# Performance work log

Hardware: AMD Instinct MI355X
Metric: run time of the kernel (lower is better)

The kernel has to match this reference:

```python
import jax, jax.numpy as jnp
import numpy as np

# ---- config (mirrors AAModel init kwargs: ns=48, nv=10, sh_lmax=1) ----
N, E, NS, NV = 100000, 60000, 48, 10
SED, DED = 32, 32          # sigma / distance embedding dims
CUTOFF = 30.0              # GaussianSmearing(0, cutoff, DED)
SQ3 = float(np.sqrt(3.0))
W1_NUMEL = NS * NS + NS * NV                                   # 2784
# layer-2 fully-connected TP path weight offsets:
#   0e(x)0e->0e, 0e(x)1o->1o, 1o(x)0e->1o, 1o(x)1o->0e, 1o(x)1o->1e
O2 = [2304, 2784, 2884, 3364, 3464]


def _mlp2(x, W1, b1, W2, b2):
    return jax.nn.relu(x @ W1 + b1) @ W2 + b2


def _seg_mean(x, idx, n):
    s = jax.ops.segment_sum(x, idx, num_segments=n)
    cnt = jax.ops.segment_sum(jnp.ones(idx.shape, x.dtype), idx, num_segments=n)
    return s / jnp.maximum(cnt, 1.0).reshape((n,) + (1,) * (x.ndim - 1))


def _forward(pos, node_sigma_emb, node_s, edge_W1, edge_b1, edge_W2, edge_b2,
             fc1_W1, fc1_b1, fc1_W2, fc1_b2, fc2_W1, fc2_b1, fc2_W2, fc2_b2,
             edge_index):
    src, dst = edge_index[0], edge_index[1]
    vec = pos[dst] - pos[src]                          # [E,3]
    d = jnp.linalg.norm(vec, axis=-1)                  # [E]
    sh1 = SQ3 * vec / (d[:, None] + 1e-8)              # l=1 SH, component norm; sh0 == 1
    # Gaussian smearing of edge distances
    offsets = jnp.linspace(0.0, CUTOFF, DED)
    coeff = -0.5 / (offsets[1] - offsets[0]) ** 2
    demb = jnp.exp(coeff * (d[:, None] - offsets) ** 2)          # [E,DED]
    edge_emb = _mlp2(jnp.concatenate([node_sigma_emb[src], demb], -1),
                     edge_W1, edge_b1, edge_W2, edge_b2)         # [E,NS]

    # ---- conv layer 1:  ns x0e  (x)  1x0e+1x1o  ->  ns x0e + nv x1o ----
    xs = node_s[src]
    ea = jnp.concatenate([edge_emb, node_s[src], node_s[dst]], -1)   # [E,3*NS]
    w = _mlp2(ea, fc1_W1, fc1_b1, fc1_W2, fc1_b2)                    # [E,2784]
    w00 = w[:, :NS * NS].reshape(-1, NS, NS)
    w01 = w[:, NS * NS:].reshape(-1, NS, NV)
    inv = 1.0 / np.sqrt(NS)
    m_s = jnp.einsum('eio,ei->eo', w00, xs) * inv                    # [E,NS]
    m_v = jnp.einsum('eio,ei->eo', w01, xs)[:, :, None] * sh1[:, None, :] * inv  # [E,NV,3]
    node_s1 = node_s + _seg_mean(m_s, dst, N)                        # residual
    node_v1 = _seg_mean(m_v, dst, N)

    # ---- conv layer 2:  ns x0e + nv x1o  (x)  1x0e+1x1o  ->  ns x0e + nv x1o + nv x1e ----
    ea2 = jnp.concatenate([edge_emb, node_s1[src], node_s1[dst]], -1)
    w2 = _mlp2(ea2, fc2_W1, fc2_b1, fc2_W2, fc2_b2)                  # [E,3464]
    w00 = w2[:, :O2[0]].reshape(-1, NS, NS)
    w01 = w2[:, O2[0]:O2[1]].reshape(-1, NS, NV)
    w10 = w2[:, O2[1]:O2[2]].reshape(-1, NV, NV)
    w11s = w2[:, O2[2]:O2[3]].reshape(-1, NV, NS)
    w11p = w2[:, O2[3]:O2[4]].reshape(-1, NV, NV)
    xs, xv = node_s1[src], node_v1[src]
    nA = 1.0 / np.sqrt(2 * NS)
    nB = 1.0 / np.sqrt(2 * NV)
    m_s = (jnp.einsum('eio,ei->eo', w00, xs) * nA
           + jnp.einsum('eio,eid,ed->eo', w11s, xv, sh1) * (nB / SQ3))
    m_v = (jnp.einsum('eio,ei->eo', w01, xs)[:, :, None] * sh1[:, None, :] * nA
           + jnp.einsum('eio,eid->eod', w10, xv) * nB)
    m_p = jnp.einsum('eio,eid->eod', w11p, jnp.cross(xv, sh1[:, None, :])) * (1.0 / np.sqrt(2.0 * NV))
    node_s2 = node_s1 + _seg_mean(m_s, dst, N)
    node_v2 = node_v1 + _seg_mean(m_v, dst, N)
    node_p = _seg_mean(m_p, dst, N)
    # final node irreps ns x0e + nv x1o + nv x1e, flattened -> [N, 108]
    return jnp.concatenate([node_s2, node_v2.reshape(N, -1), node_p.reshape(N, -1)], -1)


def setup_inputs() -> dict:
    key = jax.random.key(0)
    k = jax.random.split(key, 10)
    f32 = jnp.float32
    def lin(kk, fi, fo):
        return jax.random.normal(kk, (fi, fo), f32) / np.sqrt(fi)
    return {
        'pos': 10.0 * jax.random.normal(k[0], (N, 3), f32),
        'node_sigma_emb': jax.random.normal(k[1], (N, SED), f32),
        'node_s': jax.random.normal(k[2], (N, NS), f32),
        'edge_W1': lin(k[3], SED + DED, NS), 'edge_b1': jnp.zeros((NS,), f32),
        'edge_W2': lin(k[4], NS, NS), 'edge_b2': jnp.zeros((NS,), f32),
        'fc1_W1': lin(k[5], 3 * NS, 3 * NS), 'fc1_b1': jnp.zeros((3 * NS,), f32),
        'fc1_W2': lin(k[6], 3 * NS, W1_NUMEL), 'fc1_b2': jnp.zeros((W1_NUMEL,), f32),
        'fc2_W1': lin(k[7], 3 * NS, 3 * NS), 'fc2_b1': jnp.zeros((3 * NS,), f32),
        'fc2_W2': lin(k[8], 3 * NS, O2[-1]), 'fc2_b2': jnp.zeros((O2[-1],), f32),
        'edge_index': jax.random.randint(k[9], (2, E), 0, N, jnp.int32),
    }


def reference(pos, node_sigma_emb, node_s, edge_W1, edge_b1, edge_W2, edge_b2,
              fc1_W1, fc1_b1, fc1_W2, fc1_b2, fc2_W1, fc2_b1, fc2_W2, fc2_b2,
              edge_index):
    return _forward(pos, node_sigma_emb, node_s, edge_W1, edge_b1, edge_W2, edge_b2,
                    fc1_W1, fc1_b1, fc1_W2, fc1_b2, fc2_W1, fc2_b1, fc2_W2, fc2_b2,
                    edge_index)
```

## Files before the change

### kernel.cpp

```cpp
#include <hip/hip_runtime.h>
#include <math.h>


constexpr float SQ3f = 1.7320508075688772f;
constexpr float INV1 = 0.14433756729740643f;
constexpr float NAc  = 0.10206207261596575f;
constexpr float NBc  = 0.22360679774997896f;
constexpr float C20  = 0.22360679774997896f;
constexpr float RATIO= 1.2649110640673518f;
constexpr float DSP  = 30.0f/31.0f;
constexpr float GCOEF= -0.5f/(DSP*DSP);

typedef __attribute__((ext_vector_type(8))) short bf16x8;
typedef __attribute__((ext_vector_type(4))) float f32x4;

__device__ __forceinline__ unsigned short f2bf(float x) {
    unsigned u = __builtin_bit_cast(unsigned, x);
    u += 0x7fffu + ((u >> 16) & 1u);
    return (unsigned short)(u >> 16);
}

__device__ __forceinline__ int colmap(int layer, int t, int lm) {
    if (layer == 0) return t*16 + lm;
    if (layer == 1) {
        if (t < 144) { const int og=t/48, i=t-og*48; return i*48 + og*16 + lm; }
        const int i = t-144; return (lm<10) ? 2304 + i*10 + lm : -1;
    }
    if (t < 144) { const int og=t/48, i=t-og*48; return i*48 + og*16 + lm; }
    if (t < 174) { const int s=t-144, og=s/10, i=s-og*10; return 2884 + i*48 + og*16 + lm; }
    if (t < 222) { const int i=t-174; return (lm<10) ? 2304 + i*10 + lm : -1; }
    if (t < 232) { const int i=t-222; return (lm<10) ? 2784 + i*10 + lm : -1; }
    { const int i=t-232; return (lm<10) ? 3364 + i*10 + lm : -1; }
}

__global__ __launch_bounds__(256)
void cvt_swz(const float* __restrict__ W, const float* __restrict__ bias,
             short* __restrict__ Wsw, int ncol, int ntile, int layer)
{
    const int gid = blockIdx.x*256 + threadIdx.x;
    const int g = gid >> 6, lane = gid & 63;
    if (g >= ntile*5) return;
    const int tile = g/5, ks = g - tile*5;
    const int c  = colmap(layer, tile, lane & 15);
    const int k0 = ks*32 + (lane >> 4)*8;
    union { uint4 u4; unsigned short h[8]; } pk;
    #pragma unroll
    for (int j=0;j<8;j++) {
        const int k = k0 + j;
        float v = 0.f;
        if (c >= 0) {
            if (k < 144)       v = W[(size_t)k*ncol + c];
            else if (k == 144) v = bias[c];
        }
        pk.h[j] = f2bf(v);
    }
    *(uint4*)&Wsw[((size_t)g*64 + lane)*8] = pk.u4;
}

__global__ __launch_bounds__(256)
void edge_kernel(const float* __restrict__ pos, const float* __restrict__ sigma,
                 const int* __restrict__ ei,
                 const float* __restrict__ W1, const float* __restrict__ b1,
                 const float* __restrict__ W2, const float* __restrict__ b2,
                 float* __restrict__ edge_emb, float* __restrict__ sh1buf,
                 int* __restrict__ deg, int E)
{
    __shared__ float inl[4][64];
    __shared__ float hidl[4][48];
    const int w    = threadIdx.x >> 6;
    const int lane = threadIdx.x & 63;
    const int e    = blockIdx.x*4 + w;
    const bool valid = (e < E);
    const int ec = valid ? e : 0;
    const int src = ei[ec], dst = ei[E+ec];
    const float vx = pos[dst*3+0]-pos[src*3+0];
    const float vy = pos[dst*3+1]-pos[src*3+1];
    const float vz = pos[dst*3+2]-pos[src*3+2];
    const float d  = sqrtf(vx*vx+vy*vy+vz*vz);
    const float si = SQ3f/(d+1e-8f);
    const float s0 = vx*si, s1 = vy*si, s2 = vz*si;
    if (lane < 32) {
        inl[w][lane] = sigma[src*32+lane];
    } else {
        const float off  = (float)(lane-32)*DSP;
        const float diff = d - off;
        inl[w][lane] = expf(GCOEF*diff*diff);
    }
    __syncthreads();
    if (lane < 48) {
        float a = b1[lane];
        #pragma unroll 8
        for (int j=0;j<64;j++) a = fmaf(inl[w][j], W1[j*48+lane], a);
        hidl[w][lane] = fmaxf(a, 0.f);
    }
    __syncthreads();
    if (valid) {
        if (lane < 48) {
            float a = b2[lane];
            #pragma unroll 8
            for (int j=0;j<48;j++) a = fmaf(hidl[w][j], W2[j*48+lane], a);
            edge_emb[e*48+lane] = a;
        }
        if (lane == 0) atomicAdd(&deg[dst], 1);
        if (lane < 3)  sh1buf[e*4+lane] = (lane==0)?s0:((lane==1)?s1:s2);
    }
}

__device__ __forceinline__ void load_bfrag(const short* __restrict__ Wsw,
                                           int tile, int lane, bf16x8 (&b)[5]) {
    #pragma unroll
    for (int ks=0; ks<5; ks++)
        b[ks] = *(const bf16x8*)&Wsw[((size_t)(tile*5+ks)*64 + lane)*8];
}

template<typename F>
__device__ __forceinline__ void region1(const short* __restrict__ Wsw, int base,
                                        int count, int lane,
                                        const bf16x8 (&ag)[4][5], F&& upd)
{
    bf16x8 bc[5], bn[5];
    load_bfrag(Wsw, base, lane, bc);
    for (int i=0; i<count; ++i) {
        if (i+1 < count) load_bfrag(Wsw, base+i+1, lane, bn);
        f32x4 a[4];
        #pragma unroll
        for (int mt=0; mt<4; mt++) a[mt] = (f32x4){0.f,0.f,0.f,0.f};
        #pragma unroll
        for (int ks=0; ks<5; ks++)
            #pragma unroll
            for (int mt=0; mt<4; mt++)
                a[mt] = __builtin_amdgcn_mfma_f32_16x16x32_bf16(ag[mt][ks], bc[ks], a[mt], 0,0,0);
        upd(i, a);
        #pragma unroll
        for (int ks=0; ks<5; ks++) bc[ks] = bn[ks];
    }
}

template<int LAYER>
__global__ __launch_bounds__(256)
void conv_kernel(const float* __restrict__ edge_emb, const float* __restrict__ sh1buf,
                 const int* __restrict__ ei,
                 const float* __restrict__ sin_, const float* __restrict__ vin,
                 const short* __restrict__ W1sw, const short* __restrict__ W2sw,
                 float* __restrict__ outS, float* __restrict__ outV, int E)
{
    __shared__ __align__(16) short pool[64*192];
    __shared__ __align__(16) float xsT[48][68];
    __shared__ float sh1l[64][4];
    __shared__ int   srcl[64], dstl[64];
    __shared__ __align__(16) float xvT[LAYER==2 ? 30 : 1][68];
    __shared__ __align__(16) float uT [LAYER==2 ? 10 : 1][68];
    __shared__ __align__(16) float cvT[LAYER==2 ? 30 : 1][68];

    const int t  = threadIdx.x;
    const int eb = blockIdx.x * 64;

    if (t < 64) {
        const int ge = eb + t; const int gc = (ge < E) ? ge : (E-1);
        srcl[t] = ei[gc]; dstl[t] = ei[E+gc];
    }
    {
        const int e = t >> 2, k = t & 3;
        const int ge = eb + e; const int gc = (ge<E)?ge:(E-1);
        sh1l[e][k] = sh1buf[gc*4 + k];
    }
    __syncthreads();

    for (int p = t; p < 64*24; p += 256) {
        const int m = p / 24, s = p - m*24;
        const int k0 = s*8;
        float vals[8] = {0.f,0.f,0.f,0.f,0.f,0.f,0.f,0.f};
        if (k0 < 48) {
            const int ge = eb + m; const int gc = (ge<E)?ge:(E-1);
            const float4 a = *(const float4*)&edge_emb[gc*48 + k0];
            const float4 b = *(const float4*)&edge_emb[gc*48 + k0 + 4];
            vals[0]=a.x; vals[1]=a.y; vals[2]=a.z; vals[3]=a.w;
            vals[4]=b.x; vals[5]=b.y; vals[6]=b.z; vals[7]=b.w;
        } else if (k0 < 96) {
            const float4 a = *(const float4*)&sin_[srcl[m]*48 + (k0-48)];
            const float4 b = *(const float4*)&sin_[srcl[m]*48 + (k0-48) + 4];
            vals[0]=a.x; vals[1]=a.y; vals[2]=a.z; vals[3]=a.w;
            vals[4]=b.x; vals[5]=b.y; vals[6]=b.z; vals[7]=b.w;
            #pragma unroll
            for (int j=0;j<8;j++) xsT[k0-48+j][m] = vals[j];
        } else if (k0 < 144) {
            const float4 a = *(const float4*)&sin_[dstl[m]*48 + (k0-96)];
            const float4 b = *(const float4*)&sin_[dstl[m]*48 + (k0-96) + 4];
            vals[0]=a.x; vals[1]=a.y; vals[2]=a.z; vals[3]=a.w;
            vals[4]=b.x; vals[5]=b.y; vals[6]=b.z; vals[7]=b.w;
        } else if (k0 == 144) {
            vals[0] = 1.f;
        }
        union { uint4 u4; unsigned short h[8]; } pk;
        #pragma unroll
        for (int j=0;j<8;j++) pk.h[j] = f2bf(vals[j]);
        *(uint4*)&pool[m*192 + ((s ^ (m&7))*8)] = pk.u4;
    }
    if (LAYER==2) {
        for (int p=t; p<640; p+=256) {
            const int i = p >> 6, e = p & 63;
            const float x0 = vin[srcl[e]*30 + i*3+0];
            const float x1 = vin[srcl[e]*30 + i*3+1];
            const float x2 = vin[srcl[e]*30 + i*3+2];
            const float h0=sh1l[e][0], h1=sh1l[e][1], h2=sh1l[e][2];
            xvT[i*3+0][e]=x0; xvT[i*3+1][e]=x1; xvT[i*3+2][e]=x2;
            uT[i][e] = x0*h0 + x1*h1 + x2*h2;
            cvT[i*3+0][e] = x1*h2 - x2*h1;
            cvT[i*3+1][e] = x2*h0 - x0*h2;
            cvT[i*3+2][e] = x0*h1 - x1*h0;
        }
    }
    __syncthreads();

    const int wv = t >> 6, lane = t & 63;
    const int lm = lane & 15, lk = lane >> 4, lk4 = lk*4;

    {
        bf16x8 af[4][5];
        #pragma unroll
        for (int mt=0; mt<4; mt++) {
            const int m = mt*16 + lm;
            #pragma unroll
            for (int ks=0; ks<5; ks++)
                af[mt][ks] = *(const bf16x8*)&pool[m*192 + (((ks*4+lk) ^ (m&7))*8)];
        }
        f32x4 acc[3][4];
        #pragma unroll
        for (int j=0; j<3; j++) {
            const int nt = wv + j*4;
            if (nt < 9) {
                bf16x8 bw[5];
                load_bfrag(W1sw, nt, lane, bw);
                #pragma unroll
                for (int mt=0; mt<4; mt++) acc[j][mt] = (f32x4){0.f,0.f,0.f,0.f};
                #pragma unroll
                for (int ks=0; ks<5; ks++)
                    #pragma unroll
                    for (int mt=0; mt<4; mt++)
                        acc[j][mt] = __builtin_amdgcn_mfma_f32_16x16x32_bf16(af[mt][ks], bw[ks], acc[j][mt], 0,0,0);
            }
        }
        __syncthreads();
        #pragma unroll
        for (int j=0; j<3; j++) {
            const int nt = wv + j*4;
            if (nt < 9) {
                const int c = nt*16 + lm;
                #pragma unroll
                for (int mt=0; mt<4; mt++)
                    #pragma unroll
                    for (int r=0; r<4; r++) {
                        const int m = mt*16 + lk4 + r;
                        pool[m*192 + (((c>>3) ^ (m&7))*8) + (c&7)] = (short)f2bf(fmaxf(acc[j][mt][r], 0.f));
                    }
            }
        }
        if (t < 128) {
            const int m = t >> 1, s = 18 + (t & 1);
            union { uint4 u4; unsigned short h[8]; } pk;
            pk.u4.x = pk.u4.y = pk.u4.z = pk.u4.w = 0u;
            if (s == 18) pk.h[0] = f2bf(1.f);
            *(uint4*)&pool[m*192 + ((s ^ (m&7))*8)] = pk.u4;
        }
    }
    __syncthreads();

    bf16x8 ag[4][5];
    #pragma unroll
    for (int mt=0; mt<4; mt++) {
        const int m = mt*16 + lm;
        #pragma unroll
        for (int ks=0; ks<5; ks++)
            ag[mt][ks] = *(const bf16x8*)&pool[m*192 + (((ks*4+lk) ^ (m&7))*8)];
    }

    if (wv < 3) {
        float ms[4][4] = {};
        region1(W2sw, wv*48, 48, lane, ag, [&](int i, const f32x4 (&a)[4]) {
            #pragma unroll
            for (int mt=0; mt<4; mt++) {
                const f32x4 x = *(const f32x4*)&xsT[i][mt*16 + lk4];
                #pragma unroll
                for (int r=0;r<4;r++) ms[mt][r] = fmaf(a[mt][r], x[r], ms[mt][r]);
            }
        });
        if (LAYER==2) {
            region1(W2sw, 144 + wv*10, 10, lane, ag, [&](int i, const f32x4 (&a)[4]) {
                #pragma unroll
                for (int mt=0; mt<4; mt++) {
                    const f32x4 u = *(const f32x4*)&uT[i][mt*16 + lk4];
                    #pragma unroll
                    for (int r=0;r<4;r++) ms[mt][r] = fmaf(a[mt][r]*RATIO, u[r], ms[mt][r]);
                }
            });
        }
        const float scale = (LAYER==1) ? INV1 : NAc;
        const int   strd  = (LAYER==1) ? 48 : 108;
        const int o = wv*16 + lm;
        #pragma unroll
        for (int mt=0; mt<4; mt++)
            #pragma unroll
            for (int r=0;r<4;r++) {
                const int e = mt*16 + lk4 + r;
                if (eb+e < E) unsafeAtomicAdd(&outS[(size_t)dstl[e]*strd + o], ms[mt][r]*scale);
            }
    } else {
        float vc[4][4] = {};
        region1(W2sw, (LAYER==1) ? 144 : 174, 48, lane, ag, [&](int i, const f32x4 (&a)[4]) {
            #pragma unroll
            for (int mt=0; mt<4; mt++) {
                const f32x4 x = *(const f32x4*)&xsT[i][mt*16 + lk4];
                #pragma unroll
                for (int r=0;r<4;r++) vc[mt][r] = fmaf(a[mt][r], x[r], vc[mt][r]);
            }
        });
        if (LAYER==1) {
            if (lm < 10) {
                #pragma unroll
                for (int mt=0; mt<4; mt++)
                    #pragma unroll
                    for (int r=0;r<4;r++) {
                        const int e = mt*16 + lk4 + r;
                        if (eb+e < E) {
                            const float v = vc[mt][r]*INV1;
                            #pragma unroll
                            for (int d=0; d<3; d++)
                                unsafeAtomicAdd(&outV[(size_t)dstl[e]*30 + lm*3 + d], v*sh1l[e][d]);
                        }
                    }
            }
        } else {
            {
                float m3[4][4][3] = {};
                region1(W2sw, 222, 10, lane, ag, [&](int i, const f32x4 (&a)[4]) {
                    #pragma unroll
                    for (int d=0; d<3; d++)
                        #pragma unroll
                        for (int mt=0; mt<4; mt++) {
                            const f32x4 x = *(const f32x4*)&xvT[i*3+d][mt*16 + lk4];
                            #pragma unroll
                            for (int r=0;r<4;r++) m3[mt][r][d] = fmaf(a[mt][r], x[r], m3[mt][r][d]);
                        }
                });
                if (lm < 10) {
                    #pragma unroll
                    for (int mt=0; mt<4; mt++)
                        #pragma unroll
                        for (int r=0;r<4;r++) {
                            const int e = mt*16 + lk4 + r;
                            if (eb+e < E) {
                                const float v = vc[mt][r]*NAc;
                                #pragma unroll
                                for (int d=0; d<3; d++)
                                    unsafeAtomicAdd(&outS[(size_t)dstl[e]*108 + 48 + lm*3 + d],
                                                    v*sh1l[e][d] + m3[mt][r][d]*NBc);
                            }
                        }
                }
            }
            {
                float m3[4][4][3] = {};
                region1(W2sw, 232, 10, lane, ag, [&](int i, const f32x4 (&a)[4]) {
                    #pragma unroll
                    for (int d=0; d<3; d++)
                        #pragma unroll
                        for (int mt=0; mt<4; mt++) {
                            const f32x4 x = *(const f32x4*)&cvT[i*3+d][mt*16 + lk4];
                            #pragma unroll
                            for (int r=0;r<4;r++) m3[mt][r][d] = fmaf(a[mt][r], x[r], m3[mt][r][d]);
                        }
                });
                if (lm < 10) {
                    #pragma unroll
                    for (int mt=0; mt<4; mt++)
                        #pragma unroll
                        for (int r=0;r<4;r++) {
                            const int e = mt*16 + lk4 + r;
                            if (eb+e < E) {
                                #pragma unroll
                                for (int d=0; d<3; d++)
                                    unsafeAtomicAdd(&outS[(size_t)dstl[e]*108 + 78 + lm*3 + d],
                                                    m3[mt][r][d]*C20);
                            }
                        }
                }
            }
        }
    }
}

__global__ __launch_bounds__(256)
void fin1_kernel(const float* __restrict__ node_s, const int* __restrict__ deg,
                 float* __restrict__ s1, float* __restrict__ v1, int Nn)
{
    const int p = blockIdx.x*256 + threadIdx.x;
    const int totS = Nn*48;
    if (p < totS) {
        const int n = p/48;
        const int dgi = deg[n];
        const float dg = (float)(dgi > 1 ? dgi : 1);
        s1[p] = node_s[p] + s1[p]/dg;
    } else {
        const int q = p - totS;
        if (q < Nn*30) {
            const int n = q/30;
            const int dgi = deg[n];
            const float dg = (float)(dgi > 1 ? dgi : 1);
            v1[q] = v1[q]/dg;
        }
    }
}

__global__ __launch_bounds__(256)
void fin2_kernel(const float* __restrict__ s1, const float* __restrict__ v1,
                 const int* __restrict__ deg, float* __restrict__ out, int Nn)
{
    const int p = blockIdx.x*256 + threadIdx.x;
    if (p >= Nn*108) return;
    const int n = p/108, c = p - n*108;
    const int dgi = deg[n];
    const float dg = (float)(dgi > 1 ? dgi : 1);
    const float acc = out[p]/dg;
    if (c < 48)      out[p] = s1[n*48+c] + acc;
    else if (c < 78) out[p] = v1[n*30 + (c-48)] + acc;
    else             out[p] = acc;
}

extern "C" void kernel_launch(void* const* d_in, const int* in_sizes, int n_in,
                              void* d_out, int out_size, void* d_ws, size_t ws_size,
                              hipStream_t stream)
{
    const float* pos    = (const float*)d_in[0];
    const float* sigma  = (const float*)d_in[1];
    const float* node_s = (const float*)d_in[2];
    const float* eW1  = (const float*)d_in[3];
    const float* eb1  = (const float*)d_in[4];
    const float* eW2  = (const float*)d_in[5];
    const float* eb2  = (const float*)d_in[6];
    const float* f1W1 = (const float*)d_in[7];
    const float* f1b1 = (const float*)d_in[8];
    const float* f1W2 = (const float*)d_in[9];
    const float* f1b2 = (const float*)d_in[10];
    const float* f2W1 = (const float*)d_in[11];
    const float* f2b1 = (const float*)d_in[12];
    const float* f2W2 = (const float*)d_in[13];
    const float* f2b2 = (const float*)d_in[14];
    const int*   ei   = (const int*)d_in[15];
    const int Nn = in_sizes[0]/3;
    const int E  = in_sizes[15]/2;
    float* out = (float*)d_out;

    char* ws = (char*)d_ws;
    float* edge_emb = (float*)ws;  ws += (size_t)E*48*sizeof(float);
    float* sh1buf   = (float*)ws;  ws += (size_t)E*4*sizeof(float);
    float* s1       = (float*)ws;  ws += (size_t)Nn*48*sizeof(float);
    float* v1       = (float*)ws;  ws += (size_t)Nn*30*sizeof(float);
    int*   deg      = (int*)ws;    ws += (size_t)Nn*sizeof(int);
    short* W1sw     = (short*)ws;  ws += (size_t)9*5*64*8*sizeof(short);
    short* W2sw     = (short*)ws;  ws += (size_t)242*5*64*8*sizeof(short);

    hipMemsetAsync(s1,  0, (size_t)Nn*48*sizeof(float), stream);
    hipMemsetAsync(v1,  0, (size_t)Nn*30*sizeof(float), stream);
    hipMemsetAsync(deg, 0, (size_t)Nn*sizeof(int),      stream);
    hipMemsetAsync(out, 0, (size_t)Nn*108*sizeof(float), stream);

    edge_kernel<<<(E+3)/4, 256, 0, stream>>>(pos, sigma, ei, eW1, eb1, eW2, eb2,
                                             edge_emb, sh1buf, deg, E);

    cvt_swz<<<(9*5*64+255)/256,   256, 0, stream>>>(f1W1, f1b1, W1sw, 144, 9, 0);
    cvt_swz<<<(192*5*64+255)/256, 256, 0, stream>>>(f1W2, f1b2, W2sw, 2784, 192, 1);

    conv_kernel<1><<<(E+63)/64, 256, 0, stream>>>(edge_emb, sh1buf, ei, node_s, nullptr,
                                                  W1sw, W2sw, s1, v1, E);
    fin1_kernel<<<((size_t)Nn*78 + 255)/256, 256, 0, stream>>>(node_s, deg, s1, v1, Nn);

    cvt_swz<<<(9*5*64+255)/256,   256, 0, stream>>>(f2W1, f2b1, W1sw, 144, 9, 0);
    cvt_swz<<<(242*5*64+255)/256, 256, 0, stream>>>(f2W2, f2b2, W2sw, 3464, 242, 2);

    conv_kernel<2><<<(E+63)/64, 256, 0, stream>>>(edge_emb, sh1buf, ei, s1, v1,
                                                  W1sw, W2sw, out, nullptr, E);
    fin2_kernel<<<((size_t)Nn*108 + 255)/256, 256, 0, stream>>>(s1, v1, deg, out, Nn);
}
```

Measured before the change: 519.7 us.

## Split conv edge tile across wave pairs, halving A-fragment registers per wave

The second GEMM stage previously had each of 4 waves own all 64 edges (4 M-tiles) and one output group (three scalar groups plus one vector group). Now the waves form two pairs and each wave covers 32 edges (2 M-tiles). Pair 0 handles scalar groups 0 and 1, and pair 1 handles scalar group 2 plus the vector paths. This halves the A-fragment and accumulator registers per wave, which may improve occupancy or reduce spills. The cost is that each wave now streams twice as many B-tiles from global memory, with fewer MFMAs to amortise each load.

```diff
diff --git a/kernel.cpp b/kernel.cpp
--- a/kernel.cpp
+++ b/kernel.cpp
@@ -113,24 +113,29 @@
         b[ks] = *(const bf16x8*)&Wsw[((size_t)(tile*5+ks)*64 + lane)*8];
 }
 
+__device__ __forceinline__ void mfma5(const bf16x8 (&ag)[2][5], const bf16x8 (&b)[5],
+                                      f32x4& a0, f32x4& a1) {
+    a0 = (f32x4){0.f,0.f,0.f,0.f};
+    a1 = (f32x4){0.f,0.f,0.f,0.f};
+    #pragma unroll
+    for (int ks=0; ks<5; ks++) {
+        a0 = __builtin_amdgcn_mfma_f32_16x16x32_bf16(ag[0][ks], b[ks], a0, 0,0,0);
+        a1 = __builtin_amdgcn_mfma_f32_16x16x32_bf16(ag[1][ks], b[ks], a1, 0,0,0);
+    }
+}
+
 template<typename F>
 __device__ __forceinline__ void region1(const short* __restrict__ Wsw, int base,
                                         int count, int lane,
-                                        const bf16x8 (&ag)[4][5], F&& upd)
+                                        const bf16x8 (&ag)[2][5], F&& upd)
 {
     bf16x8 bc[5], bn[5];
     load_bfrag(Wsw, base, lane, bc);
     for (int i=0; i<count; ++i) {
         if (i+1 < count) load_bfrag(Wsw, base+i+1, lane, bn);
-        f32x4 a[4];
-        #pragma unroll
-        for (int mt=0; mt<4; mt++) a[mt] = (f32x4){0.f,0.f,0.f,0.f};
-        #pragma unroll
-        for (int ks=0; ks<5; ks++)
-            #pragma unroll
-            for (int mt=0; mt<4; mt++)
-                a[mt] = __builtin_amdgcn_mfma_f32_16x16x32_bf16(ag[mt][ks], bc[ks], a[mt], 0,0,0);
-        upd(i, a);
+        f32x4 a0, a1;
+        mfma5(ag, bc, a0, a1);
+        upd(i, a0, a1);
         #pragma unroll
         for (int ks=0; ks<5; ks++) bc[ks] = bn[ks];
     }
@@ -265,64 +270,79 @@
     }
     __syncthreads();
 
-    bf16x8 ag[4][5];
+    const int pair = wv >> 1;
+    const int half = wv & 1;
+    const int e0b  = half*32;
+    const int col0 = e0b + lk4;
+
+    bf16x8 ag[2][5];
     #pragma unroll
-    for (int mt=0; mt<4; mt++) {
-        const int m = mt*16 + lm;
+    for (int mtl=0; mtl<2; mtl++) {
+        const int m = e0b + mtl*16 + lm;
         #pragma unroll
         for (int ks=0; ks<5; ks++)
-            ag[mt][ks] = *(const bf16x8*)&pool[m*192 + (((ks*4+lk) ^ (m&7))*8)];
-    }
-
-    if (wv < 3) {
-        float ms[4][4] = {};
-        region1(W2sw, wv*48, 48, lane, ag, [&](int i, const f32x4 (&a)[4]) {
+            ag[mtl][ks] = *(const bf16x8*)&pool[m*192 + (((ks*4+lk) ^ (m&7))*8)];
+    }
+
+    const float sScale = (LAYER==1) ? INV1 : NAc;
+    const int   sStrd  = (LAYER==1) ? 48 : 108;
+
+    auto do_og = [&](int og) {
+        float ms[2][4] = {{0.f,0.f,0.f,0.f},{0.f,0.f,0.f,0.f}};
+        region1(W2sw, og*48, 48, lane, ag, [&](int i, f32x4 a0, f32x4 a1) {
+            const f32x4 x0 = *(const f32x4*)&xsT[i][col0];
+            const f32x4 x1 = *(const f32x4*)&xsT[i][col0+16];
             #pragma unroll
-            for (int mt=0; mt<4; mt++) {
-                const f32x4 x = *(const f32x4*)&xsT[i][mt*16 + lk4];
-                #pragma unroll
-                for (int r=0;r<4;r++) ms[mt][r] = fmaf(a[mt][r], x[r], ms[mt][r]);
+            for (int r=0;r<4;r++) {
+                ms[0][r] = fmaf(a0[r], x0[r], ms[0][r]);
+                ms[1][r] = fmaf(a1[r], x1[r], ms[1][r]);
             }
         });
         if (LAYER==2) {
-            region1(W2sw, 144 + wv*10, 10, lane, ag, [&](int i, const f32x4 (&a)[4]) {
+            region1(W2sw, 144 + og*10, 10, lane, ag, [&](int i, f32x4 a0, f32x4 a1) {
+                const f32x4 u0 = *(const f32x4*)&uT[i][col0];
+                const f32x4 u1 = *(const f32x4*)&uT[i][col0+16];
                 #pragma unroll
-                for (int mt=0; mt<4; mt++) {
-                    const f32x4 u = *(const f32x4*)&uT[i][mt*16 + lk4];
-                    #pragma unroll
-                    for (int r=0;r<4;r++) ms[mt][r] = fmaf(a[mt][r]*RATIO, u[r], ms[mt][r]);
+                for (int r=0;r<4;r++) {
+                    ms[0][r] = fmaf(a0[r]*RATIO, u0[r], ms[0][r]);
+                    ms[1][r] = fmaf(a1[r]*RATIO, u1[r], ms[1][r]);
                 }
             });
         }
-        const float scale = (LAYER==1) ? INV1 : NAc;
-        const int   strd  = (LAYER==1) ? 48 : 108;
-        const int o = wv*16 + lm;
-        #pragma unroll
-        for (int mt=0; mt<4; mt++)
+        const int o = og*16 + lm;
+        #pragma unroll
+        for (int mtl=0; mtl<2; mtl++)
             #pragma unroll
             for (int r=0;r<4;r++) {
-                const int e = mt*16 + lk4 + r;
-                if (eb+e < E) unsafeAtomicAdd(&outS[(size_t)dstl[e]*strd + o], ms[mt][r]*scale);
-            }
+                const int e = e0b + mtl*16 + lk4 + r;
+                if (eb+e < E) unsafeAtomicAdd(&outS[(size_t)dstl[e]*sStrd + o], ms[mtl][r]*sScale);
+            }
+    };
+
+    if (pair == 0) {
+        do_og(0);
+        do_og(1);
     } else {
-        float vc[4][4] = {};
-        region1(W2sw, (LAYER==1) ? 144 : 174, 48, lane, ag, [&](int i, const f32x4 (&a)[4]) {
+        do_og(2);
+        float vc[2][4] = {{0.f,0.f,0.f,0.f},{0.f,0.f,0.f,0.f}};
+        region1(W2sw, (LAYER==1) ? 144 : 174, 48, lane, ag, [&](int i, f32x4 a0, f32x4 a1) {
+            const f32x4 x0 = *(const f32x4*)&xsT[i][col0];
+            const f32x4 x1 = *(const f32x4*)&xsT[i][col0+16];
             #pragma unroll
-            for (int mt=0; mt<4; mt++) {
-                const f32x4 x = *(const f32x4*)&xsT[i][mt*16 + lk4];
-                #pragma unroll
-                for (int r=0;r<4;r++) vc[mt][r] = fmaf(a[mt][r], x[r], vc[mt][r]);
+            for (int r=0;r<4;r++) {
+                vc[0][r] = fmaf(a0[r], x0[r], vc[0][r]);
+                vc[1][r] = fmaf(a1[r], x1[r], vc[1][r]);
             }
         });
         if (LAYER==1) {
             if (lm < 10) {
                 #pragma unroll
-                for (int mt=0; mt<4; mt++)
+                for (int mtl=0; mtl<2; mtl++)
                     #pragma unroll
                     for (int r=0;r<4;r++) {
-                        const int e = mt*16 + lk4 + r;
+                        const int e = e0b + mtl*16 + lk4 + r;
                         if (eb+e < E) {
-                            const float v = vc[mt][r]*INV1;
+                            const float v = vc[mtl][r]*INV1;
                             #pragma unroll
                             for (int d=0; d<3; d++)
                                 unsafeAtomicAdd(&outV[(size_t)dstl[e]*30 + lm*3 + d], v*sh1l[e][d]);
@@ -331,56 +351,60 @@
             }
         } else {
             {
-                float m3[4][4][3] = {};
-                region1(W2sw, 222, 10, lane, ag, [&](int i, const f32x4 (&a)[4]) {
-                    #pragma unroll
-                    for (int d=0; d<3; d++)
+                float m3[2][4][3] = {};
+                region1(W2sw, 222, 10, lane, ag, [&](int i, f32x4 a0, f32x4 a1) {
+                    #pragma unroll
+                    for (int d=0; d<3; d++) {
+                        const f32x4 x0 = *(const f32x4*)&xvT[i*3+d][col0];
+                        const f32x4 x1 = *(const f32x4*)&xvT[i*3+d][col0+16];
                         #pragma unroll
-                        for (int mt=0; mt<4; mt++) {
-                            const f32x4 x = *(const f32x4*)&xvT[i*3+d][mt*16 + lk4];
-                            #pragma unroll
-                            for (int r=0;r<4;r++) m3[mt][r][d] = fmaf(a[mt][r], x[r], m3[mt][r][d]);
+                        for (int r=0;r<4;r++) {
+                            m3[0][r][d] = fmaf(a0[r], x0[r], m3[0][r][d]);
+                            m3[1][r][d] = fmaf(a1[r], x1[r], m3[1][r][d]);
                         }
+                    }
                 });
                 if (lm < 10) {
                     #pragma unroll
-                    for (int mt=0; mt<4; mt++)
+                    for (int mtl=0; mtl<2; mtl++)
                         #pragma unroll
                         for (int r=0;r<4;r++) {
-                            const int e = mt*16 + lk4 + r;
+                            const int e = e0b + mtl*16 + lk4 + r;
                             if (eb+e < E) {
-                                const float v = vc[mt][r]*NAc;
+                                const float v = vc[mtl][r]*NAc;
                                 #pragma unroll
                                 for (int d=0; d<3; d++)
                                     unsafeAtomicAdd(&outS[(size_t)dstl[e]*108 + 48 + lm*3 + d],
-                                                    v*sh1l[e][d] + m3[mt][r][d]*NBc);
+                                                    v*sh1l[e][d] + m3[mtl][r][d]*NBc);
                             }
                         }
                 }
             }
             {
-                float m3[4][4][3] = {};
-                region1(W2sw, 232, 10, lane, ag, [&](int i, const f32x4 (&a)[4]) {
-                    #pragma unroll
-                    for (int d=0; d<3; d++)
+                float m3[2][4][3] = {};
+                region1(W2sw, 232, 10, lane, ag, [&](int i, f32x4 a0, f32x4 a1) {
+                    #pragma unroll
+                    for (int d=0; d<3; d++) {
+                        const f32x4 x0 = *(const f32x4*)&cvT[i*3+d][col0];
+                        const f32x4 x1 = *(const f32x4*)&cvT[i*3+d][col0+16];
                         #pragma unroll
-                        for (int mt=0; mt<4; mt++) {
-                            const f32x4 x = *(const f32x4*)&cvT[i*3+d][mt*16 + lk4];
-                            #pragma unroll
-                            for (int r=0;r<4;r++) m3[mt][r][d] = fmaf(a[mt][r], x[r], m3[mt][r][d]);
+                        for (int r=0;r<4;r++) {
+                            m3[0][r][d] = fmaf(a0[r], x0[r], m3[0][r][d]);
+                            m3[1][r][d] = fmaf(a1[r], x1[r], m3[1][r][d]);
                         }
+                    }
                 });
                 if (lm < 10) {
                     #pragma unroll
-                    for (int mt=0; mt<4; mt++)
+                    for (int mtl=0; mtl<2; mtl++)
                         #pragma unroll
                         for (int r=0;r<4;r++) {
-                            const int e = mt*16 + lk4 + r;
+                            const int e = e0b + mtl*16 + lk4 + r;
                             if (eb+e < E) {
                                 #pragma unroll
                                 for (int d=0; d<3; d++)
                                     unsafeAtomicAdd(&outS[(size_t)dstl[e]*108 + 78 + lm*3 + d],
-                                                    m3[mt][r][d]*C20);
+                                                    m3[mtl][r][d]*C20);
                             }
                         }
                 }
```

After: 519.9 us. Within noise of the previous version (+0.0%).

## Partition second GEMM by edge rows per wave with LDS double-buffered weight staging

Applied to the files above, without the earlier changes.

The second fused GEMM is reorganized so each wave owns 16 edge rows and iterates over all weight column tiles, instead of each wave owning a column region over all 64 edges. Weight tiles are staged into shared memory with asynchronous global_load_lds in double-buffered pairs shared by the four waves, rather than each wave streaming its own fragments from global memory. The xs transpose is stored as bf16, and the first GEMM is split into two halves to reduce register pressure. The trade-off is a block-wide barrier every two tiles and more serialized MFMA chains per wave.

```diff
diff --git a/kernel.cpp b/kernel.cpp
--- a/kernel.cpp
+++ b/kernel.cpp
@@ -18,6 +18,9 @@
     unsigned u = __builtin_bit_cast(unsigned, x);
     u += 0x7fffu + ((u >> 16) & 1u);
     return (unsigned short)(u >> 16);
+}
+__device__ __forceinline__ float bf2f(unsigned short h) {
+    return __builtin_bit_cast(float, ((unsigned)h) << 16);
 }
 
 __device__ __forceinline__ int colmap(int layer, int t, int lm) {
@@ -113,29 +116,6 @@
         b[ks] = *(const bf16x8*)&Wsw[((size_t)(tile*5+ks)*64 + lane)*8];
 }
 
-template<typename F>
-__device__ __forceinline__ void region1(const short* __restrict__ Wsw, int base,
-                                        int count, int lane,
-                                        const bf16x8 (&ag)[4][5], F&& upd)
-{
-    bf16x8 bc[5], bn[5];
-    load_bfrag(Wsw, base, lane, bc);
-    for (int i=0; i<count; ++i) {
-        if (i+1 < count) load_bfrag(Wsw, base+i+1, lane, bn);
-        f32x4 a[4];
-        #pragma unroll
-        for (int mt=0; mt<4; mt++) a[mt] = (f32x4){0.f,0.f,0.f,0.f};
-        #pragma unroll
-        for (int ks=0; ks<5; ks++)
-            #pragma unroll
-            for (int mt=0; mt<4; mt++)
-                a[mt] = __builtin_amdgcn_mfma_f32_16x16x32_bf16(ag[mt][ks], bc[ks], a[mt], 0,0,0);
-        upd(i, a);
-        #pragma unroll
-        for (int ks=0; ks<5; ks++) bc[ks] = bn[ks];
-    }
-}
-
 template<int LAYER>
 __global__ __launch_bounds__(256)
 void conv_kernel(const float* __restrict__ edge_emb, const float* __restrict__ sh1buf,
@@ -144,13 +124,16 @@
                  const short* __restrict__ W1sw, const short* __restrict__ W2sw,
                  float* __restrict__ outS, float* __restrict__ outV, int E)
 {
+    constexpr int NT = (LAYER==1) ? 192 : 242;
+    constexpr int NG = NT/2;
+
     __shared__ __align__(16) short pool[64*192];
-    __shared__ __align__(16) float xsT[48][68];
+    __shared__ __align__(16) unsigned short xsTb[48][64];
     __shared__ float sh1l[64][4];
     __shared__ int   srcl[64], dstl[64];
-    __shared__ __align__(16) float xvT[LAYER==2 ? 30 : 1][68];
-    __shared__ __align__(16) float uT [LAYER==2 ? 10 : 1][68];
-    __shared__ __align__(16) float cvT[LAYER==2 ? 30 : 1][68];
+    __shared__ __align__(16) float xvT[LAYER==2 ? 30 : 1][64];
+    __shared__ __align__(16) float uT [LAYER==2 ? 10 : 1][64];
+    __shared__ __align__(16) float cvT[LAYER==2 ? 30 : 1][64];
 
     const int t  = threadIdx.x;
     const int eb = blockIdx.x * 64;
@@ -181,8 +164,6 @@
             const float4 b = *(const float4*)&sin_[srcl[m]*48 + (k0-48) + 4];
             vals[0]=a.x; vals[1]=a.y; vals[2]=a.z; vals[3]=a.w;
             vals[4]=b.x; vals[5]=b.y; vals[6]=b.z; vals[7]=b.w;
-            #pragma unroll
-            for (int j=0;j<8;j++) xsT[k0-48+j][m] = vals[j];
         } else if (k0 < 144) {
             const float4 a = *(const float4*)&sin_[dstl[m]*48 + (k0-96)];
             const float4 b = *(const float4*)&sin_[dstl[m]*48 + (k0-96) + 4];
@@ -195,6 +176,10 @@
         #pragma unroll
         for (int j=0;j<8;j++) pk.h[j] = f2bf(vals[j]);
         *(uint4*)&pool[m*192 + ((s ^ (m&7))*8)] = pk.u4;
+        if (k0 >= 48 && k0 < 96) {
+            #pragma unroll
+            for (int j=0;j<8;j++) xsTb[k0-48+j][m] = pk.h[j];
+        }
     }
     if (LAYER==2) {
         for (int p=t; p<640; p+=256) {
@@ -215,16 +200,16 @@
     const int wv = t >> 6, lane = t & 63;
     const int lm = lane & 15, lk = lane >> 4, lk4 = lk*4;
 
+    f32x4 aa[3][2], ab[3][2];
     {
-        bf16x8 af[4][5];
-        #pragma unroll
-        for (int mt=0; mt<4; mt++) {
+        bf16x8 af[2][5];
+        #pragma unroll
+        for (int mt=0; mt<2; mt++) {
             const int m = mt*16 + lm;
             #pragma unroll
             for (int ks=0; ks<5; ks++)
                 af[mt][ks] = *(const bf16x8*)&pool[m*192 + (((ks*4+lk) ^ (m&7))*8)];
         }
-        f32x4 acc[3][4];
         #pragma unroll
         for (int j=0; j<3; j++) {
             const int nt = wv + j*4;
@@ -232,157 +217,192 @@
                 bf16x8 bw[5];
                 load_bfrag(W1sw, nt, lane, bw);
                 #pragma unroll
-                for (int mt=0; mt<4; mt++) acc[j][mt] = (f32x4){0.f,0.f,0.f,0.f};
+                for (int mt=0; mt<2; mt++) aa[j][mt] = (f32x4){0.f,0.f,0.f,0.f};
                 #pragma unroll
                 for (int ks=0; ks<5; ks++)
                     #pragma unroll
-                    for (int mt=0; mt<4; mt++)
-                        acc[j][mt] = __builtin_amdgcn_mfma_f32_16x16x32_bf16(af[mt][ks], bw[ks], acc[j][mt], 0,0,0);
-            }
-        }
-        __syncthreads();
+                    for (int mt=0; mt<2; mt++)
+                        aa[j][mt] = __builtin_amdgcn_mfma_f32_16x16x32_bf16(af[mt][ks], bw[ks], aa[j][mt], 0,0,0);
+            }
+        }
+        #pragma unroll
+        for (int mt=0; mt<2; mt++) {
+            const int m = (mt+2)*16 + lm;
+            #pragma unroll
+            for (int ks=0; ks<5; ks++)
+                af[mt][ks] = *(const bf16x8*)&pool[m*192 + (((ks*4+lk) ^ (m&7))*8)];
+        }
         #pragma unroll
         for (int j=0; j<3; j++) {
             const int nt = wv + j*4;
             if (nt < 9) {
-                const int c = nt*16 + lm;
-                #pragma unroll
-                for (int mt=0; mt<4; mt++)
+                bf16x8 bw[5];
+                load_bfrag(W1sw, nt, lane, bw);
+                #pragma unroll
+                for (int mt=0; mt<2; mt++) ab[j][mt] = (f32x4){0.f,0.f,0.f,0.f};
+                #pragma unroll
+                for (int ks=0; ks<5; ks++)
                     #pragma unroll
-                    for (int r=0; r<4; r++) {
-                        const int m = mt*16 + lk4 + r;
-                        pool[m*192 + (((c>>3) ^ (m&7))*8) + (c&7)] = (short)f2bf(fmaxf(acc[j][mt][r], 0.f));
-                    }
-            }
-        }
-        if (t < 128) {
-            const int m = t >> 1, s = 18 + (t & 1);
-            union { uint4 u4; unsigned short h[8]; } pk;
-            pk.u4.x = pk.u4.y = pk.u4.z = pk.u4.w = 0u;
-            if (s == 18) pk.h[0] = f2bf(1.f);
-            *(uint4*)&pool[m*192 + ((s ^ (m&7))*8)] = pk.u4;
-        }
-    }
-    __syncthreads();
-
-    bf16x8 ag[4][5];
+                    for (int mt=0; mt<2; mt++)
+                        ab[j][mt] = __builtin_amdgcn_mfma_f32_16x16x32_bf16(af[mt][ks], bw[ks], ab[j][mt], 0,0,0);
+            }
+        }
+    }
+    __syncthreads();
     #pragma unroll
-    for (int mt=0; mt<4; mt++) {
-        const int m = mt*16 + lm;
+    for (int j=0; j<3; j++) {
+        const int nt = wv + j*4;
+        if (nt < 9) {
+            const int c = nt*16 + lm;
+            #pragma unroll
+            for (int mt=0; mt<4; mt++) {
+                const f32x4 v = (mt<2) ? aa[j][mt] : ab[j][mt-2];
+                #pragma unroll
+                for (int r=0; r<4; r++) {
+                    const int m = mt*16 + lk4 + r;
+                    pool[m*192 + (((c>>3) ^ (m&7))*8) + (c&7)] = (short)f2bf(fmaxf(v[r], 0.f));
+                }
+            }
+        }
+    }
+    if (t < 128) {
+        const int m = t >> 1, s = 18 + (t & 1);
+        union { uint4 u4; unsigned short h[8]; } pk;
+        pk.u4.x = pk.u4.y = pk.u4.z = pk.u4.w = 0u;
+        if (s == 18) pk.h[0] = f2bf(1.f);
+        *(uint4*)&pool[m*192 + ((s ^ (m&7))*8)] = pk.u4;
+    }
+    __syncthreads();
+
+    bf16x8 ag[5];
+    {
+        const int m = wv*16 + lm;
         #pragma unroll
         for (int ks=0; ks<5; ks++)
-            ag[mt][ks] = *(const bf16x8*)&pool[m*192 + (((ks*4+lk) ^ (m&7))*8)];
-    }
-
-    if (wv < 3) {
-        float ms[4][4] = {};
-        region1(W2sw, wv*48, 48, lane, ag, [&](int i, const f32x4 (&a)[4]) {
-            #pragma unroll
-            for (int mt=0; mt<4; mt++) {
-                const f32x4 x = *(const f32x4*)&xsT[i][mt*16 + lk4];
-                #pragma unroll
-                for (int r=0;r<4;r++) ms[mt][r] = fmaf(a[mt][r], x[r], ms[mt][r]);
-            }
+            ag[ks] = *(const bf16x8*)&pool[m*192 + (((ks*4+lk) ^ (m&7))*8)];
+    }
+    __syncthreads();
+
+    auto STAGE = [&](int bufsel, int g) {
+        const char* gsrc = (const char*)W2sw + (size_t)g*10240;
+        char* lbase = (char*)pool + bufsel*10240;
+        for (int c = wv; c < 10; c += 4) {
+            __builtin_amdgcn_global_load_lds(
+                (const __attribute__((address_space(1))) void*)(gsrc + c*1024 + lane*16),
+                (__attribute__((address_space(3))) void*)(lbase + c*1024),
+                16, 0, 0);
+        }
+    };
+
+    int gstage = 1, cur = 0;
+    STAGE(0, 0);
+    __syncthreads();
+
+    const int col0 = wv*16 + lk4;
+
+    auto runpairs = [&](int count, auto&& upd) {
+        for (int i = 0; i < count; i += 2) {
+            if (gstage < NG) { STAGE(cur^1, gstage); ++gstage; }
+            const short* tb = pool + cur*5120;
+            #pragma unroll
+            for (int s = 0; s < 2; ++s) {
+                bf16x8 bf_[5];
+                #pragma unroll
+                for (int ks=0; ks<5; ks++)
+                    bf_[ks] = *(const bf16x8*)&tb[s*2560 + ks*512 + lane*8];
+                f32x4 a = (f32x4){0.f,0.f,0.f,0.f};
+                #pragma unroll
+                for (int ks=0; ks<5; ks++)
+                    a = __builtin_amdgcn_mfma_f32_16x16x32_bf16(ag[ks], bf_[ks], a, 0,0,0);
+                upd(i+s, a);
+            }
+            __syncthreads();
+            cur ^= 1;
+        }
+    };
+
+    float ms0[4]={0,0,0,0}, ms1[4]={0,0,0,0}, ms2[4]={0,0,0,0}, vc[4]={0,0,0,0};
+    float m3[4][3] = {};
+    float p3[4][3] = {};
+
+    auto upd_ms = [&](float (&ms)[4], int i, const f32x4& a, float scale) {
+        const ushort4 xw = *(const ushort4*)&xsTb[i][col0];
+        ms[0] = fmaf(a[0]*scale, bf2f(xw.x), ms[0]);
+        ms[1] = fmaf(a[1]*scale, bf2f(xw.y), ms[1]);
+        ms[2] = fmaf(a[2]*scale, bf2f(xw.z), ms[2]);
+        ms[3] = fmaf(a[3]*scale, bf2f(xw.w), ms[3]);
+    };
+
+    runpairs(48, [&](int i, const f32x4& a){ upd_ms(ms0, i, a, 1.f); });
+    runpairs(48, [&](int i, const f32x4& a){ upd_ms(ms1, i, a, 1.f); });
+    runpairs(48, [&](int i, const f32x4& a){ upd_ms(ms2, i, a, 1.f); });
+    if (LAYER==2) {
+        runpairs(10, [&](int i, const f32x4& a){
+            const f32x4 u = *(const f32x4*)&uT[i][col0];
+            #pragma unroll
+            for (int r=0;r<4;r++) ms0[r] = fmaf(a[r]*RATIO, u[r], ms0[r]);
         });
-        if (LAYER==2) {
-            region1(W2sw, 144 + wv*10, 10, lane, ag, [&](int i, const f32x4 (&a)[4]) {
-                #pragma unroll
-                for (int mt=0; mt<4; mt++) {
-                    const f32x4 u = *(const f32x4*)&uT[i][mt*16 + lk4];
-                    #pragma unroll
-                    for (int r=0;r<4;r++) ms[mt][r] = fmaf(a[mt][r]*RATIO, u[r], ms[mt][r]);
-                }
-            });
-        }
-        const float scale = (LAYER==1) ? INV1 : NAc;
-        const int   strd  = (LAYER==1) ? 48 : 108;
-        const int o = wv*16 + lm;
-        #pragma unroll
-        for (int mt=0; mt<4; mt++)
-            #pragma unroll
-            for (int r=0;r<4;r++) {
-                const int e = mt*16 + lk4 + r;
-                if (eb+e < E) unsafeAtomicAdd(&outS[(size_t)dstl[e]*strd + o], ms[mt][r]*scale);
-            }
-    } else {
-        float vc[4][4] = {};
-        region1(W2sw, (LAYER==1) ? 144 : 174, 48, lane, ag, [&](int i, const f32x4 (&a)[4]) {
-            #pragma unroll
-            for (int mt=0; mt<4; mt++) {
-                const f32x4 x = *(const f32x4*)&xsT[i][mt*16 + lk4];
-                #pragma unroll
-                for (int r=0;r<4;r++) vc[mt][r] = fmaf(a[mt][r], x[r], vc[mt][r]);
-            }
+        runpairs(10, [&](int i, const f32x4& a){
+            const f32x4 u = *(const f32x4*)&uT[i][col0];
+            #pragma unroll
+            for (int r=0;r<4;r++) ms1[r] = fmaf(a[r]*RATIO, u[r], ms1[r]);
         });
-        if (LAYER==1) {
-            if (lm < 10) {
-                #pragma unroll
-                for (int mt=0; mt<4; mt++)
-                    #pragma unroll
-                    for (int r=0;r<4;r++) {
-                        const int e = mt*16 + lk4 + r;
-                        if (eb+e < E) {
-                            const float v = vc[mt][r]*INV1;
-                            #pragma unroll
-                            for (int d=0; d<3; d++)
-                                unsafeAtomicAdd(&outV[(size_t)dstl[e]*30 + lm*3 + d], v*sh1l[e][d]);
-                        }
-                    }
-            }
-        } else {
-            {
-                float m3[4][4][3] = {};
-                region1(W2sw, 222, 10, lane, ag, [&](int i, const f32x4 (&a)[4]) {
+        runpairs(10, [&](int i, const f32x4& a){
+            const f32x4 u = *(const f32x4*)&uT[i][col0];
+            #pragma unroll
+            for (int r=0;r<4;r++) ms2[r] = fmaf(a[r]*RATIO, u[r], ms2[r]);
+        });
+    }
+    runpairs(48, [&](int i, const f32x4& a){ upd_ms(vc, i, a, 1.f); });
+    if (LAYER==2) {
+        runpairs(10, [&](int i, const f32x4& a){
+            #pragma unroll
+            for (int d=0; d<3; d++) {
+                const f32x4 x = *(const f32x4*)&xvT[i*3+d][col0];
+                #pragma unroll
+                for (int r=0;r<4;r++) m3[r][d] = fmaf(a[r], x[r], m3[r][d]);
+            }
+        });
+        runpairs(10, [&](int i, const f32x4& a){
+            #pragma unroll
+            for (int d=0; d<3; d++) {
+                const f32x4 x = *(const f32x4*)&cvT[i*3+d][col0];
+                #pragma unroll
+                for (int r=0;r<4;r++) p3[r][d] = fmaf(a[r], x[r], p3[r][d]);
+            }
+        });
+    }
+
+    const float sScale = (LAYER==1) ? INV1 : NAc;
+    const int   sStrd  = (LAYER==1) ? 48 : 108;
+    #pragma unroll
+    for (int r=0;r<4;r++) {
+        const int e = wv*16 + lk4 + r;
+        if (eb+e < E) {
+            const size_t base = (size_t)dstl[e]*sStrd;
+            unsafeAtomicAdd(&outS[base + 0*16 + lm], ms0[r]*sScale);
+            unsafeAtomicAdd(&outS[base + 1*16 + lm], ms1[r]*sScale);
+            unsafeAtomicAdd(&outS[base + 2*16 + lm], ms2[r]*sScale);
+        }
+    }
+    if (lm < 10) {
+        #pragma unroll
+        for (int r=0;r<4;r++) {
+            const int e = wv*16 + lk4 + r;
+            if (eb+e < E) {
+                if (LAYER==1) {
+                    const float v = vc[r]*INV1;
                     #pragma unroll
                     for (int d=0; d<3; d++)
-                        #pragma unroll
-                        for (int mt=0; mt<4; mt++) {
-                            const f32x4 x = *(const f32x4*)&xvT[i*3+d][mt*16 + lk4];
-                            #pragma unroll
-                            for (int r=0;r<4;r++) m3[mt][r][d] = fmaf(a[mt][r], x[r], m3[mt][r][d]);
-                        }
-                });
-                if (lm < 10) {
+                        unsafeAtomicAdd(&outV[(size_t)dstl[e]*30 + lm*3 + d], v*sh1l[e][d]);
+                } else {
+                    const float v = vc[r]*NAc;
+                    const size_t base = (size_t)dstl[e]*108;
                     #pragma unroll
-                    for (int mt=0; mt<4; mt++)
-                        #pragma unroll
-                        for (int r=0;r<4;r++) {
-                            const int e = mt*16 + lk4 + r;
-                            if (eb+e < E) {
-                                const float v = vc[mt][r]*NAc;
-                                #pragma unroll
-                                for (int d=0; d<3; d++)
-                                    unsafeAtomicAdd(&outS[(size_t)dstl[e]*108 + 48 + lm*3 + d],
-                                                    v*sh1l[e][d] + m3[mt][r][d]*NBc);
-                            }
-                        }
-                }
-            }
-            {
-                float m3[4][4][3] = {};
-                region1(W2sw, 232, 10, lane, ag, [&](int i, const f32x4 (&a)[4]) {
-                    #pragma unroll
-                    for (int d=0; d<3; d++)
-                        #pragma unroll
-                        for (int mt=0; mt<4; mt++) {
-                            const f32x4 x = *(const f32x4*)&cvT[i*3+d][mt*16 + lk4];
-                            #pragma unroll
-                            for (int r=0;r<4;r++) m3[mt][r][d] = fmaf(a[mt][r], x[r], m3[mt][r][d]);
-                        }
-                });
-                if (lm < 10) {
-                    #pragma unroll
-                    for (int mt=0; mt<4; mt++)
-                        #pragma unroll
-                        for (int r=0;r<4;r++) {
-                            const int e = mt*16 + lk4 + r;
-                            if (eb+e < E) {
-                                #pragma unroll
-                                for (int d=0; d<3; d++)
-                                    unsafeAtomicAdd(&outS[(size_t)dstl[e]*108 + 78 + lm*3 + d],
-                                                    m3[mt][r][d]*C20);
-                            }
-                        }
+                    for (int d=0; d<3; d++) {
+                        unsafeAtomicAdd(&outS[base + 48 + lm*3 + d], v*sh1l[e][d] + m3[r][d]*NBc);
+                        unsafeAtomicAdd(&outS[base + 78 + lm*3 + d], p3[r][d]*C20);
+                    }
                 }
             }
         }
```

After: 494.5 us. -4.9%, faster.
